# Kernel optimization log

Hardware: AMD Instinct MI355X
Metric: run time of the kernel (lower is better)

The kernel has to match this reference:

```python
import jax, jax.numpy as jnp
import numpy as np

N_EMBD = 1024
N_HEAD = 16


def setup_inputs() -> dict:
    key = jax.random.key(0)
    ks = jax.random.split(key, 5)
    s = 0.02
    x = jax.random.normal(ks[0], (4, 2048, N_EMBD), dtype=jnp.float32)
    W_attn = jax.random.normal(ks[1], (N_EMBD, 3 * N_EMBD), dtype=jnp.float32) * s
    b_attn = jnp.zeros((3 * N_EMBD,), dtype=jnp.float32)
    W_proj = jax.random.normal(ks[2], (N_EMBD, N_EMBD), dtype=jnp.float32) * s
    b_proj = jnp.zeros((N_EMBD,), dtype=jnp.float32)
    return {"x": x, "W_attn": W_attn, "b_attn": b_attn, "W_proj": W_proj, "b_proj": b_proj}


def reference(x, W_attn, b_attn, W_proj, b_proj):
    B, T, C = x.shape
    H = N_HEAD
    D = C // H
    qkv = x @ W_attn + b_attn  # [B,T,3C]
    q, k, v = jnp.split(qkv, 3, axis=-1)
    # [B,H,T,D]
    q = q.reshape(B, T, H, D).transpose(0, 2, 1, 3)
    k = k.reshape(B, T, H, D).transpose(0, 2, 1, 3)
    v = v.reshape(B, T, H, D).transpose(0, 2, 1, 3)
    att = jnp.einsum('bhqd,bhkd->bhqk', q, k) * (1.0 / np.sqrt(D))
    causal = jnp.tril(jnp.ones((T, T), dtype=bool))
    att = jnp.where(causal[None, None], att, -jnp.inf)
    att = jax.nn.softmax(att, axis=-1)
    y = jnp.einsum('bhqk,bhkd->bhqd', att, v)
    y = y.transpose(0, 2, 1, 3).reshape(B, T, C)
    return y @ W_proj + b_proj
```

## Files before the change

kernel.cpp:

```cpp
#include <hip/hip_runtime.h>
#include <hip/hip_bf16.h>

#define B_ 4
#define T_ 2048
#define C_ 1024
#define H_ 16
#define D_ 64
#define N3_ 3072
#define M_ (B_*T_)

typedef __bf16 bf16x8 __attribute__((ext_vector_type(8)));
typedef float f32x4 __attribute__((ext_vector_type(4)));

__device__ __forceinline__ unsigned short f2bf(float f){
  __bf16 h = (__bf16)f;
  return __builtin_bit_cast(unsigned short, h);
}
__device__ __forceinline__ unsigned int pk2(float a, float b){
  return (unsigned int)f2bf(a) | ((unsigned int)f2bf(b)<<16);
}
__device__ __forceinline__ void gload_lds16(const unsigned short* g, unsigned short* l){
  __builtin_amdgcn_global_load_lds(
      (const __attribute__((address_space(1))) void*)g,
      (__attribute__((address_space(3))) void*)l, 16, 0, 0);
}

__global__ __launch_bounds__(256) void x_cvt(
    const float* __restrict__ X, unsigned short* __restrict__ Xb)
{
  const size_t i = ((size_t)blockIdx.x*256 + threadIdx.x)*8;
  float4 f0 = *(const float4*)(X+i);
  float4 f1 = *(const float4*)(X+i+4);
  uint4 w = make_uint4(pk2(f0.x,f0.y), pk2(f0.z,f0.w), pk2(f1.x,f1.y), pk2(f1.z,f1.w));
  *(uint4*)(Xb+i) = w;
}

__global__ __launch_bounds__(256) void transpose_cvt(
    const float* __restrict__ src, unsigned short* __restrict__ dst, int K, int N)
{
  __shared__ float tile[32][33];
  const int tx = threadIdx.x & 31, ty = threadIdx.x >> 5;
  const int nt = blockIdx.x * 32, kt = blockIdx.y * 32;
  #pragma unroll
  for (int i=0;i<32;i+=8) tile[ty+i][tx] = src[(size_t)(kt+ty+i)*N + nt+tx];
  __syncthreads();
  #pragma unroll
  for (int i=0;i<32;i+=8) dst[(size_t)(nt+ty+i)*K + kt+tx] = f2bf(tile[tx][ty+i]);
}

__global__ __launch_bounds__(256) void qkv_gemm(
    const unsigned short* __restrict__ Xb, const unsigned short* __restrict__ Wt,
    const float* __restrict__ bias,
    unsigned short* __restrict__ Qb, unsigned short* __restrict__ Kb,
    unsigned short* __restrict__ Vt)
{
  __shared__ __align__(16) unsigned short As[128][32];
  __shared__ __align__(16) unsigned short Bs[128][32];
  const int tid = threadIdx.x;
  const int m0 = blockIdx.y*128, n0 = blockIdx.x*128;
  const int wv = tid>>6, lane = tid&63, lm = lane&15, lq = lane>>4;
  const int wr = wv>>1, wc = wv&1;
  f32x4 acc[4][4] = {};
  const int schunk = (lane&3) ^ ((lane>>3)&3);
  const unsigned short* gA = Xb + (size_t)(m0 + wv*32 + (lane>>2))*C_ + schunk*8;
  const unsigned short* gB = Wt + (size_t)(n0 + wv*32 + (lane>>2))*C_ + schunk*8;
  unsigned short* lA0 = &As[wv*32][0];
  unsigned short* lA1 = &As[wv*32+16][0];
  unsigned short* lB0 = &Bs[wv*32][0];
  unsigned short* lB1 = &Bs[wv*32+16][0];
  const int rkey = (lm>>1)&3;
  for (int k0=0;k0<C_;k0+=32){
    __syncthreads();
    gload_lds16(gA + k0,            lA0);
    gload_lds16(gA + 16*C_ + k0,    lA1);
    gload_lds16(gB + k0,            lB0);
    gload_lds16(gB + 16*C_ + k0,    lB1);
    __syncthreads();
    bf16x8 a[4], b[4];
    #pragma unroll
    for (int mt=0;mt<4;mt++) a[mt] = *(const bf16x8*)&As[wr*64+mt*16+lm][(lq^rkey)*8];
    #pragma unroll
    for (int nt=0;nt<4;nt++) b[nt] = *(const bf16x8*)&Bs[wc*64+nt*16+lm][(lq^rkey)*8];
    #pragma unroll
    for (int mt=0;mt<4;mt++)
      #pragma unroll
      for (int nt=0;nt<4;nt++)
        acc[mt][nt] = __builtin_amdgcn_mfma_f32_16x16x32_bf16(a[mt], b[nt], acc[mt][nt], 0,0,0);
  }
  const int sel = n0>>10;
  const float qsc = (sel==0) ? 0.18033688f : 1.0f;
  #pragma unroll
  for (int mt=0;mt<4;mt++){
    const int grow = m0 + wr*64 + mt*16 + lq*4;
    const int bb = grow>>11, tt0 = grow&2047;
    #pragma unroll
    for (int nt=0;nt<4;nt++){
      const int gcol = n0 + wc*64 + nt*16 + lm;
      const int hh = (gcol>>6)&15, dd = gcol&63;
      const float bv = bias[gcol];
      if (sel==2){
        ushort4 pv;
        pv.x = f2bf(acc[mt][nt][0] + bv);
        pv.y = f2bf(acc[mt][nt][1] + bv);
        pv.z = f2bf(acc[mt][nt][2] + bv);
        pv.w = f2bf(acc[mt][nt][3] + bv);
        *(ushort4*)&Vt[ ((size_t)(bb*H_+hh)*D_ + dd)*T_ + tt0 ] = pv;
      } else {
        unsigned short* dst = (sel==0) ? Qb : Kb;
        #pragma unroll
        for (int r=0;r<4;r++)
          dst[ ((size_t)(bb*H_+hh)*T_ + tt0 + r)*D_ + dd ] = f2bf((acc[mt][nt][r] + bv)*qsc);
      }
    }
  }
}

__global__ __launch_bounds__(256, 4) void flash_attn(
    const unsigned short* __restrict__ Qb, const unsigned short* __restrict__ Kb,
    const unsigned short* __restrict__ Vt, unsigned short* __restrict__ Yb)
{
  __shared__ __align__(16) unsigned short Ks[2][64][64];
  __shared__ __align__(16) unsigned short Vs[2][64][64];
  __shared__ __align__(16) unsigned short Ps[64][64];
  const int tid = threadIdx.x;
  const int wv = tid>>6, lane = tid&63, lm = lane&15, lq = lane>>4;
  const int id = (int)blockIdx.x;
  const int bh = id & 63;
  const int qi = 31 - (id >> 6);
  const int qbase = qi*64;
  const unsigned short* Qh = Qb + (size_t)bh*T_*D_;
  const unsigned short* Kh = Kb + (size_t)bh*T_*D_;
  const unsigned short* Vh = Vt + (size_t)bh*D_*T_;
  bf16x8 aq[2];
  {
    const int q = qbase + wv*16 + lm;
    aq[0] = *(const bf16x8*)&Qh[(size_t)q*D_ + lq*8];
    aq[1] = *(const bf16x8*)&Qh[(size_t)q*D_ + 32 + lq*8];
  }
  f32x4 o[4] = {};
  float l_r[4] = {0.f,0.f,0.f,0.f};
  const int srl = lane>>3;
  const int sc  = (lane&7) ^ srl;
  const unsigned short* kg = Kh + (size_t)(wv*16 + srl)*D_ + sc*8;
  const unsigned short* vg = Vh + (size_t)(wv*16 + srl)*T_ + sc*8;
  const int keyR = lm&7;
  {
    unsigned short* lk = &Ks[0][wv*16][0];
    unsigned short* lv = &Vs[0][wv*16][0];
    gload_lds16(kg,            lk);
    gload_lds16(kg + 8*D_,     lk + 8*64);
    gload_lds16(vg,            lv);
    gload_lds16(vg + 8*T_,     lv + 8*64);
  }
  for (int j=0;j<=qi;j++){
    const int cb = j&1;
    __syncthreads();
    if (j < qi){
      unsigned short* lk = &Ks[cb^1][wv*16][0];
      unsigned short* lv = &Vs[cb^1][wv*16][0];
      gload_lds16(kg + (size_t)((j+1)*64  )*D_, lk);
      gload_lds16(kg + (size_t)((j+1)*64+8)*D_, lk + 8*64);
      gload_lds16(vg + (j+1)*64,                lv);
      gload_lds16(vg + 8*T_ + (j+1)*64,         lv + 8*64);
    }
    f32x4 s[4] = {};
    #pragma unroll
    for (int nt=0;nt<4;nt++){
      bf16x8 bk0 = *(const bf16x8*)&Ks[cb][nt*16+lm][((lq  )^keyR)*8];
      bf16x8 bk1 = *(const bf16x8*)&Ks[cb][nt*16+lm][((lq+4)^keyR)*8];
      s[nt] = __builtin_amdgcn_mfma_f32_16x16x32_bf16(aq[0], bk0, s[nt], 0,0,0);
      s[nt] = __builtin_amdgcn_mfma_f32_16x16x32_bf16(aq[1], bk1, s[nt], 0,0,0);
    }
    if (j==qi){
      const int qrow0 = wv*16 + lq*4;
      #pragma unroll
      for (int nt=0;nt<4;nt++){
        const int col = nt*16+lm;
        #pragma unroll
        for (int r=0;r<4;r++)
          s[nt][r] = (col <= qrow0+r) ? exp2f(s[nt][r]) : 0.f;
      }
    } else {
      #pragma unroll
      for (int nt=0;nt<4;nt++)
        #pragma unroll
        for (int r=0;r<4;r++)
          s[nt][r] = exp2f(s[nt][r]);
    }
    #pragma unroll
    for (int r=0;r<4;r++)
      l_r[r] += (s[0][r]+s[1][r]) + (s[2][r]+s[3][r]);
    #pragma unroll
    for (int nt=0;nt<4;nt++)
      #pragma unroll
      for (int r=0;r<4;r++){
        const int row = wv*16 + lq*4 + r;
        const int ch  = (2*nt + (lm>>3)) ^ (row&7);
        Ps[row][ch*8 + (lm&7)] = f2bf(s[nt][r]);
      }
    #pragma unroll
    for (int kc=0;kc<2;kc++){
      bf16x8 ap = *(const bf16x8*)&Ps[wv*16+lm][((kc*4+lq)^keyR)*8];
      #pragma unroll
      for (int dt=0;dt<4;dt++){
        bf16x8 bv = *(const bf16x8*)&Vs[cb][dt*16+lm][((kc*4+lq)^keyR)*8];
        o[dt] = __builtin_amdgcn_mfma_f32_16x16x32_bf16(bv, ap, o[dt], 0,0,0);
      }
    }
  }
  #pragma unroll
  for (int r=0;r<4;r++){
    float rs = l_r[r];
    rs += __shfl_xor(rs,1); rs += __shfl_xor(rs,2);
    rs += __shfl_xor(rs,4); rs += __shfl_xor(rs,8);
    l_r[r] = rs;
  }
  const int srcl = (lm>>2)<<4;
  float lv0v = __shfl(l_r[0], srcl);
  float lv1v = __shfl(l_r[1], srcl);
  float lv2v = __shfl(l_r[2], srcl);
  float lv3v = __shfl(l_r[3], srcl);
  const int rr = lm&3;
  float linv = (rr==0) ? lv0v : (rr==1) ? lv1v : (rr==2) ? lv2v : lv3v;
  linv = 1.0f/linv;
  const int bb = bh>>4, hh = bh&15;
  const int q = qbase + wv*16 + lm;
  #pragma unroll
  for (int dt=0;dt<4;dt++){
    ushort4 y;
    y.x = f2bf(o[dt][0]*linv);
    y.y = f2bf(o[dt][1]*linv);
    y.z = f2bf(o[dt][2]*linv);
    y.w = f2bf(o[dt][3]*linv);
    *(ushort4*)&Yb[ ((size_t)bb*T_ + q)*C_ + hh*64 + dt*16 + lq*4 ] = y;
  }
}

__global__ __launch_bounds__(256) void proj_gemm(
    const unsigned short* __restrict__ Yb, const unsigned short* __restrict__ Wt,
    const float* __restrict__ bias, float* __restrict__ Out)
{
  __shared__ __align__(16) unsigned short As[128][32];
  __shared__ __align__(16) unsigned short Bs[128][32];
  const int tid = threadIdx.x;
  const int m0 = blockIdx.y*128, n0 = blockIdx.x*128;
  const int wv = tid>>6, lane = tid&63, lm = lane&15, lq = lane>>4;
  const int wr = wv>>1, wc = wv&1;
  f32x4 acc[4][4] = {};
  const int schunk = (lane&3) ^ ((lane>>3)&3);
  const unsigned short* gA = Yb + (size_t)(m0 + wv*32 + (lane>>2))*C_ + schunk*8;
  const unsigned short* gB = Wt + (size_t)(n0 + wv*32 + (lane>>2))*C_ + schunk*8;
  unsigned short* lA0 = &As[wv*32][0];
  unsigned short* lA1 = &As[wv*32+16][0];
  unsigned short* lB0 = &Bs[wv*32][0];
  unsigned short* lB1 = &Bs[wv*32+16][0];
  const int rkey = (lm>>1)&3;
  for (int k0=0;k0<C_;k0+=32){
    __syncthreads();
    gload_lds16(gA + k0,            lA0);
    gload_lds16(gA + 16*C_ + k0,    lA1);
    gload_lds16(gB + k0,            lB0);
    gload_lds16(gB + 16*C_ + k0,    lB1);
    __syncthreads();
    bf16x8 a[4], b[4];
    #pragma unroll
    for (int mt=0;mt<4;mt++) a[mt] = *(const bf16x8*)&As[wr*64+mt*16+lm][(lq^rkey)*8];
    #pragma unroll
    for (int nt=0;nt<4;nt++) b[nt] = *(const bf16x8*)&Bs[wc*64+nt*16+lm][(lq^rkey)*8];
    #pragma unroll
    for (int mt=0;mt<4;mt++)
      #pragma unroll
      for (int nt=0;nt<4;nt++)
        acc[mt][nt] = __builtin_amdgcn_mfma_f32_16x16x32_bf16(a[mt], b[nt], acc[mt][nt], 0,0,0);
  }
  #pragma unroll
  for (int mt=0;mt<4;mt++){
    const int grow = m0 + wr*64 + mt*16 + lq*4;
    #pragma unroll
    for (int nt=0;nt<4;nt++){
      const int gcol = n0 + wc*64 + nt*16 + lm;
      const float bv = bias[gcol];
      #pragma unroll
      for (int r=0;r<4;r++)
        Out[(size_t)(grow+r)*C_ + gcol] = acc[mt][nt][r] + bv;
    }
  }
}

extern "C" void kernel_launch(void* const* d_in, const int* in_sizes, int n_in,
                              void* d_out, int out_size, void* d_ws, size_t ws_size,
                              hipStream_t stream)
{
  const float* x      = (const float*)d_in[0];
  const float* W_attn = (const float*)d_in[1];
  const float* b_attn = (const float*)d_in[2];
  const float* W_proj = (const float*)d_in[3];
  const float* b_proj = (const float*)d_in[4];
  float* out = (float*)d_out;

  unsigned short* Wat = (unsigned short*)d_ws;
  unsigned short* Wpt = Wat + (size_t)N3_*C_;
  unsigned short* Xb  = Wpt + (size_t)C_*C_;
  unsigned short* Qb  = Xb  + (size_t)M_*C_;
  unsigned short* Kb  = Qb  + (size_t)M_*C_;
  unsigned short* Vt  = Kb  + (size_t)M_*C_;
  unsigned short* Yb  = Vt  + (size_t)M_*C_;
  (void)ws_size; (void)in_sizes; (void)n_in; (void)out_size;

  x_cvt        <<<dim3(M_*C_/2048),      256, 0, stream>>>(x, Xb);
  transpose_cvt<<<dim3(N3_/32, C_/32),   256, 0, stream>>>(W_attn, Wat, C_, N3_);
  transpose_cvt<<<dim3(C_/32,  C_/32),   256, 0, stream>>>(W_proj, Wpt, C_, C_);
  qkv_gemm     <<<dim3(N3_/128, M_/128), 256, 0, stream>>>(Xb, Wat, b_attn, Qb, Kb, Vt);
  flash_attn   <<<dim3(2048),            256, 0, stream>>>(Qb, Kb, Vt, Yb);
  proj_gemm    <<<dim3(C_/128, M_/128),  256, 0, stream>>>(Yb, Wpt, b_proj, out);
}
```

Before: 259.8 us.

## Swap MFMA operand order to vectorize epilogue stores and simplify softmax rowsum

Swaps the A/B operands of the MFMA in the QK GEMM epilogue for Q/K, in the attention score computation, and in the projection GEMM. Each lane then holds four consecutive columns of one row. This allows 8-byte bf16 stores for Q/K, 16-byte float4 stores for the output and bias loads, and ushort4 writes of P into shared memory. In attention, the row sum becomes a per-lane scalar reduced with two shuffles instead of a 16-lane butterfly plus a broadcast. The V path keeps the original operand order for its transposed store, which duplicates the main loop as a code-size cost.

```diff
diff --git a/kernel.cpp b/kernel.cpp
--- a/kernel.cpp
+++ b/kernel.cpp
@@ -69,47 +69,79 @@
   unsigned short* lB0 = &Bs[wv*32][0];
   unsigned short* lB1 = &Bs[wv*32+16][0];
   const int rkey = (lm>>1)&3;
-  for (int k0=0;k0<C_;k0+=32){
-    __syncthreads();
-    gload_lds16(gA + k0,            lA0);
-    gload_lds16(gA + 16*C_ + k0,    lA1);
-    gload_lds16(gB + k0,            lB0);
-    gload_lds16(gB + 16*C_ + k0,    lB1);
-    __syncthreads();
-    bf16x8 a[4], b[4];
-    #pragma unroll
-    for (int mt=0;mt<4;mt++) a[mt] = *(const bf16x8*)&As[wr*64+mt*16+lm][(lq^rkey)*8];
-    #pragma unroll
-    for (int nt=0;nt<4;nt++) b[nt] = *(const bf16x8*)&Bs[wc*64+nt*16+lm][(lq^rkey)*8];
-    #pragma unroll
-    for (int mt=0;mt<4;mt++)
-      #pragma unroll
-      for (int nt=0;nt<4;nt++)
-        acc[mt][nt] = __builtin_amdgcn_mfma_f32_16x16x32_bf16(a[mt], b[nt], acc[mt][nt], 0,0,0);
-  }
   const int sel = n0>>10;
-  const float qsc = (sel==0) ? 0.18033688f : 1.0f;
-  #pragma unroll
-  for (int mt=0;mt<4;mt++){
-    const int grow = m0 + wr*64 + mt*16 + lq*4;
-    const int bb = grow>>11, tt0 = grow&2047;
-    #pragma unroll
-    for (int nt=0;nt<4;nt++){
-      const int gcol = n0 + wc*64 + nt*16 + lm;
-      const int hh = (gcol>>6)&15, dd = gcol&63;
-      const float bv = bias[gcol];
-      if (sel==2){
+  if (sel != 2){
+    for (int k0=0;k0<C_;k0+=32){
+      __syncthreads();
+      gload_lds16(gA + k0,            lA0);
+      gload_lds16(gA + 16*C_ + k0,    lA1);
+      gload_lds16(gB + k0,            lB0);
+      gload_lds16(gB + 16*C_ + k0,    lB1);
+      __syncthreads();
+      bf16x8 a[4], b[4];
+      #pragma unroll
+      for (int mt=0;mt<4;mt++) a[mt] = *(const bf16x8*)&As[wr*64+mt*16+lm][(lq^rkey)*8];
+      #pragma unroll
+      for (int nt=0;nt<4;nt++) b[nt] = *(const bf16x8*)&Bs[wc*64+nt*16+lm][(lq^rkey)*8];
+      #pragma unroll
+      for (int mt=0;mt<4;mt++)
+        #pragma unroll
+        for (int nt=0;nt<4;nt++)
+          acc[mt][nt] = __builtin_amdgcn_mfma_f32_16x16x32_bf16(b[nt], a[mt], acc[mt][nt], 0,0,0);
+    }
+    const float qsc = (sel==0) ? 0.18033688f : 1.0f;
+    unsigned short* dst = (sel==0) ? Qb : Kb;
+    #pragma unroll
+    for (int mt=0;mt<4;mt++){
+      const int t = m0 + wr*64 + mt*16 + lm;
+      const int bb = t>>11, tt = t&2047;
+      #pragma unroll
+      for (int nt=0;nt<4;nt++){
+        const int gcol0 = n0 + wc*64 + nt*16 + lq*4;
+        const int hh = (gcol0>>6)&15, dd0 = gcol0&63;
+        const float4 bv = *(const float4*)&bias[gcol0];
+        ushort4 y;
+        y.x = f2bf((acc[mt][nt][0] + bv.x)*qsc);
+        y.y = f2bf((acc[mt][nt][1] + bv.y)*qsc);
+        y.z = f2bf((acc[mt][nt][2] + bv.z)*qsc);
+        y.w = f2bf((acc[mt][nt][3] + bv.w)*qsc);
+        *(ushort4*)&dst[ ((size_t)(bb*H_+hh)*T_ + tt)*D_ + dd0 ] = y;
+      }
+    }
+  } else {
+    for (int k0=0;k0<C_;k0+=32){
+      __syncthreads();
+      gload_lds16(gA + k0,            lA0);
+      gload_lds16(gA + 16*C_ + k0,    lA1);
+      gload_lds16(gB + k0,            lB0);
+      gload_lds16(gB + 16*C_ + k0,    lB1);
+      __syncthreads();
+      bf16x8 a[4], b[4];
+      #pragma unroll
+      for (int mt=0;mt<4;mt++) a[mt] = *(const bf16x8*)&As[wr*64+mt*16+lm][(lq^rkey)*8];
+      #pragma unroll
+      for (int nt=0;nt<4;nt++) b[nt] = *(const bf16x8*)&Bs[wc*64+nt*16+lm][(lq^rkey)*8];
+      #pragma unroll
+      for (int mt=0;mt<4;mt++)
+        #pragma unroll
+        for (int nt=0;nt<4;nt++)
+          acc[mt][nt] = __builtin_amdgcn_mfma_f32_16x16x32_bf16(a[mt], b[nt], acc[mt][nt], 0,0,0);
+    }
+    #pragma unroll
+    for (int mt=0;mt<4;mt++){
+      const int grow = m0 + wr*64 + mt*16 + lq*4;
+      const int bb = grow>>11, tt0 = grow&2047;
+      #pragma unroll
+      for (int nt=0;nt<4;nt++){
+        const int gcol = n0 + wc*64 + nt*16 + lm;
+        const int hh = (gcol>>6)&15, dd = gcol&63;
+        const float bv = bias[gcol];
         ushort4 pv;
         pv.x = f2bf(acc[mt][nt][0] + bv);
         pv.y = f2bf(acc[mt][nt][1] + bv);
         pv.z = f2bf(acc[mt][nt][2] + bv);
         pv.w = f2bf(acc[mt][nt][3] + bv);
         *(ushort4*)&Vt[ ((size_t)(bb*H_+hh)*D_ + dd)*T_ + tt0 ] = pv;
-      } else {
-        unsigned short* dst = (sel==0) ? Qb : Kb;
-        #pragma unroll
-        for (int r=0;r<4;r++)
-          dst[ ((size_t)(bb*H_+hh)*T_ + tt0 + r)*D_ + dd ] = f2bf((acc[mt][nt][r] + bv)*qsc);
       }
     }
   }
@@ -138,7 +170,7 @@
     aq[1] = *(const bf16x8*)&Qh[(size_t)q*D_ + 32 + lq*8];
   }
   f32x4 o[4] = {};
-  float l_r[4] = {0.f,0.f,0.f,0.f};
+  float l_acc = 0.f;
   const int srl = lane>>3;
   const int sc  = (lane&7) ^ srl;
   const unsigned short* kg = Kh + (size_t)(wv*16 + srl)*D_ + sc*8;
@@ -152,6 +184,8 @@
     gload_lds16(vg,            lv);
     gload_lds16(vg + 8*T_,     lv + 8*64);
   }
+  unsigned short* prow = &Ps[wv*16+lm][0];
+  const int c0 = lq>>1, hOff = (lq&1)*4;
   for (int j=0;j<=qi;j++){
     const int cb = j&1;
     __syncthreads();
@@ -168,18 +202,16 @@
     for (int nt=0;nt<4;nt++){
       bf16x8 bk0 = *(const bf16x8*)&Ks[cb][nt*16+lm][((lq  )^keyR)*8];
       bf16x8 bk1 = *(const bf16x8*)&Ks[cb][nt*16+lm][((lq+4)^keyR)*8];
-      s[nt] = __builtin_amdgcn_mfma_f32_16x16x32_bf16(aq[0], bk0, s[nt], 0,0,0);
-      s[nt] = __builtin_amdgcn_mfma_f32_16x16x32_bf16(aq[1], bk1, s[nt], 0,0,0);
+      s[nt] = __builtin_amdgcn_mfma_f32_16x16x32_bf16(bk0, aq[0], s[nt], 0,0,0);
+      s[nt] = __builtin_amdgcn_mfma_f32_16x16x32_bf16(bk1, aq[1], s[nt], 0,0,0);
     }
     if (j==qi){
-      const int qrow0 = wv*16 + lq*4;
-      #pragma unroll
-      for (int nt=0;nt<4;nt++){
-        const int col = nt*16+lm;
+      const int qloc = wv*16 + lm;
+      #pragma unroll
+      for (int nt=0;nt<4;nt++)
         #pragma unroll
         for (int r=0;r<4;r++)
-          s[nt][r] = (col <= qrow0+r) ? exp2f(s[nt][r]) : 0.f;
-      }
+          s[nt][r] = (nt*16 + lq*4 + r <= qloc) ? exp2f(s[nt][r]) : 0.f;
     } else {
       #pragma unroll
       for (int nt=0;nt<4;nt++)
@@ -187,17 +219,18 @@
         for (int r=0;r<4;r++)
           s[nt][r] = exp2f(s[nt][r]);
     }
-    #pragma unroll
-    for (int r=0;r<4;r++)
-      l_r[r] += (s[0][r]+s[1][r]) + (s[2][r]+s[3][r]);
-    #pragma unroll
-    for (int nt=0;nt<4;nt++)
-      #pragma unroll
-      for (int r=0;r<4;r++){
-        const int row = wv*16 + lq*4 + r;
-        const int ch  = (2*nt + (lm>>3)) ^ (row&7);
-        Ps[row][ch*8 + (lm&7)] = f2bf(s[nt][r]);
-      }
+    l_acc += ((s[0][0]+s[0][1])+(s[0][2]+s[0][3])) + ((s[1][0]+s[1][1])+(s[1][2]+s[1][3]))
+           + ((s[2][0]+s[2][1])+(s[2][2]+s[2][3])) + ((s[3][0]+s[3][1])+(s[3][2]+s[3][3]));
+    #pragma unroll
+    for (int nt=0;nt<4;nt++){
+      const int ch = (nt*2 + c0) ^ keyR;
+      ushort4 pw;
+      pw.x = f2bf(s[nt][0]);
+      pw.y = f2bf(s[nt][1]);
+      pw.z = f2bf(s[nt][2]);
+      pw.w = f2bf(s[nt][3]);
+      *(ushort4*)&prow[ch*8 + hOff] = pw;
+    }
     #pragma unroll
     for (int kc=0;kc<2;kc++){
       bf16x8 ap = *(const bf16x8*)&Ps[wv*16+lm][((kc*4+lq)^keyR)*8];
@@ -208,21 +241,9 @@
       }
     }
   }
-  #pragma unroll
-  for (int r=0;r<4;r++){
-    float rs = l_r[r];
-    rs += __shfl_xor(rs,1); rs += __shfl_xor(rs,2);
-    rs += __shfl_xor(rs,4); rs += __shfl_xor(rs,8);
-    l_r[r] = rs;
-  }
-  const int srcl = (lm>>2)<<4;
-  float lv0v = __shfl(l_r[0], srcl);
-  float lv1v = __shfl(l_r[1], srcl);
-  float lv2v = __shfl(l_r[2], srcl);
-  float lv3v = __shfl(l_r[3], srcl);
-  const int rr = lm&3;
-  float linv = (rr==0) ? lv0v : (rr==1) ? lv1v : (rr==2) ? lv2v : lv3v;
-  linv = 1.0f/linv;
+  l_acc += __shfl_xor(l_acc, 16);
+  l_acc += __shfl_xor(l_acc, 32);
+  const float linv = 1.0f / l_acc;
   const int bb = bh>>4, hh = bh&15;
   const int q = qbase + wv*16 + lm;
   #pragma unroll
@@ -271,18 +292,21 @@
     for (int mt=0;mt<4;mt++)
       #pragma unroll
       for (int nt=0;nt<4;nt++)
-        acc[mt][nt] = __builtin_amdgcn_mfma_f32_16x16x32_bf16(a[mt], b[nt], acc[mt][nt], 0,0,0);
+        acc[mt][nt] = __builtin_amdgcn_mfma_f32_16x16x32_bf16(b[nt], a[mt], acc[mt][nt], 0,0,0);
   }
   #pragma unroll
   for (int mt=0;mt<4;mt++){
-    const int grow = m0 + wr*64 + mt*16 + lq*4;
+    const int t = m0 + wr*64 + mt*16 + lm;
     #pragma unroll
     for (int nt=0;nt<4;nt++){
-      const int gcol = n0 + wc*64 + nt*16 + lm;
-      const float bv = bias[gcol];
-      #pragma unroll
-      for (int r=0;r<4;r++)
-        Out[(size_t)(grow+r)*C_ + gcol] = acc[mt][nt][r] + bv;
+      const int gcol0 = n0 + wc*64 + nt*16 + lq*4;
+      const float4 bv = *(const float4*)&bias[gcol0];
+      float4 y;
+      y.x = acc[mt][nt][0] + bv.x;
+      y.y = acc[mt][nt][1] + bv.y;
+      y.z = acc[mt][nt][2] + bv.z;
+      y.w = acc[mt][nt][3] + bv.w;
+      *(float4*)&Out[(size_t)t*C_ + gcol0] = y;
     }
   }
 }
```

Result: slower. 280.7 us (+8.0%).
